# Kernel tuning notes

Hardware: AMD Instinct MI355X
Metric: run time of the kernel (lower is better)

Reference implementation:

```python
import jax, jax.numpy as jnp
import numpy as np

TOP_K = 2


def setup_inputs() -> dict:
    key = jax.random.key(0)
    ks = jax.random.split(key, 5)
    B, S, H, E, I = 2, 1024, 1024, 16, 1024
    scale = 1.0 / np.sqrt(H)
    return {
        "hidden_states": jax.random.normal(ks[0], (B, S, H), dtype=jnp.float32),
        "router_w": jax.random.normal(ks[1], (E, H), dtype=jnp.float32) * scale,   # nn.Linear(H,E).weight
        "gate_w": jax.random.normal(ks[2], (E, I, H), dtype=jnp.float32) * scale,  # per-expert Linear(H,I).weight
        "up_w": jax.random.normal(ks[3], (E, I, H), dtype=jnp.float32) * scale,
        "down_w": jax.random.normal(ks[4], (E, H, I), dtype=jnp.float32) * (1.0 / np.sqrt(I)),
    }


def reference(hidden_states, router_w, gate_w, up_w, down_w):
    orig_shape = hidden_states.shape
    x = hidden_states.reshape(-1, orig_shape[-1])  # [T, H]
    T = x.shape[0]
    E = router_w.shape[0]

    # Router: sigmoid -> top-k -> normalize
    logits = jnp.einsum("th,eh->te", x, router_w)           # [T, E]
    scores = jax.nn.sigmoid(logits)
    weights, indices = jax.lax.top_k(scores, TOP_K)         # [T, K]
    weights = weights / (weights.sum(axis=-1, keepdims=True) + 1e-20)

    # Dense per-token-per-expert combine weight (0 for unrouted pairs) ==
    # exact math of the torch gather/index_add loop.
    w_full = jnp.zeros((T, E), dtype=x.dtype).at[
        jnp.arange(T)[:, None], indices
    ].add(weights)                                          # [T, E]

    # Expert MLPs (SwiGLU) computed for all experts, zero-weighted combine.
    g = jax.nn.silu(jnp.einsum("th,eih->tei", x, gate_w))   # [T, E, I]
    u = jnp.einsum("th,eih->tei", x, up_w)                  # [T, E, I]
    out = jnp.einsum("te,tei,ehi->th", w_full, g * u, down_w)  # [T, H]
    return out.reshape(orig_shape)
```

## Files before the change

### kernel.cpp

```cpp
#include <hip/hip_runtime.h>
#include <stdint.h>

#define T_TOK 2048
#define H_DIM 1024
#define E_NUM 16
#define I_DIM 1024
#define TOTAL_ROWS (2 * T_TOK)
#define CPAD 16

typedef short bf16x8 __attribute__((ext_vector_type(8)));
typedef float f32x4 __attribute__((ext_vector_type(4)));

__device__ __forceinline__ void async_copy16(const void* g, void* l) {
  __builtin_amdgcn_global_load_lds(
      (const __attribute__((address_space(1))) void*)g,
      (__attribute__((address_space(3))) void*)l, 16, 0, 0);
}

__device__ __forceinline__ uint32_t f2bf(float f) {
  uint32_t u = __float_as_uint(f);
  return (u + 0x7FFFu + ((u >> 16) & 1u)) >> 16;
}
__device__ __forceinline__ uint32_t pk2bf(float lo, float hi) {
  return f2bf(lo) | (f2bf(hi) << 16);
}

__global__ __launch_bounds__(256) void router_kernel(
    const float* __restrict__ x, const float* __restrict__ rw,
    uint16_t* __restrict__ xbf, int* __restrict__ counts,
    int* __restrict__ tokens, float* __restrict__ wts) {
  const int t = blockIdx.x * 4 + (threadIdx.x >> 6);
  const int lane = threadIdx.x & 63;

  float4 xv[4];
  float acc[E_NUM];
#pragma unroll
  for (int e = 0; e < E_NUM; ++e) acc[e] = 0.f;

#pragma unroll
  for (int rep = 0; rep < 4; ++rep) {
    const int h0 = rep * 256 + lane * 4;
    xv[rep] = *(const float4*)(x + (size_t)t * H_DIM + h0);
    uint2 p;
    p.x = pk2bf(xv[rep].x, xv[rep].y);
    p.y = pk2bf(xv[rep].z, xv[rep].w);
    *(uint2*)(xbf + (size_t)t * H_DIM + h0) = p;
  }

#pragma unroll
  for (int e = 0; e < E_NUM; ++e) {
#pragma unroll
    for (int rep = 0; rep < 4; ++rep) {
      const float4 rv = *(const float4*)(rw + (size_t)e * H_DIM + rep * 256 + lane * 4);
      acc[e] += xv[rep].x * rv.x + xv[rep].y * rv.y + xv[rep].z * rv.z +
                xv[rep].w * rv.w;
    }
  }

#pragma unroll
  for (int e = 0; e < E_NUM; ++e) {
    float v = acc[e];
#pragma unroll
    for (int off = 32; off > 0; off >>= 1) v += __shfl_xor(v, off);
    acc[e] = v;
  }

  if (lane < 2) {
    float s[E_NUM];
#pragma unroll
    for (int e = 0; e < E_NUM; ++e) s[e] = 1.f / (1.f + expf(-acc[e]));
    int i1 = 0;
    float v1 = s[0];
#pragma unroll
    for (int e = 1; e < E_NUM; ++e)
      if (s[e] > v1) { v1 = s[e]; i1 = e; }
    int i2 = -1;
    float v2 = -1.f;
#pragma unroll
    for (int e = 0; e < E_NUM; ++e)
      if (e != i1 && s[e] > v2) { v2 = s[e]; i2 = e; }
    const float inv = 1.f / (v1 + v2 + 1e-20f);
    const int pe = (lane == 0) ? i1 : i2;
    const float pw = ((lane == 0) ? v1 : v2) * inv;
    const int slot = atomicAdd(&counts[pe * CPAD], 1);
    tokens[pe * T_TOK + slot] = t;
    wts[pe * T_TOK + slot] = pw;
  }
}

__global__ void offsets_kernel(const int* __restrict__ counts,
                               int* __restrict__ offsets) {
  if (threadIdx.x == 0) {
    int a = 0;
    for (int e = 0; e < E_NUM; ++e) {
      offsets[e] = a;
      a += counts[e * CPAD];
    }
    offsets[E_NUM] = a;
  }
}


__global__ __launch_bounds__(512, 4) void gemm1_kernel(
    const uint16_t* __restrict__ xbf, const float* __restrict__ gate,
    const float* __restrict__ up, const int* __restrict__ counts,
    const int* __restrict__ offsets, const int* __restrict__ tokens,
    const float* __restrict__ wts, uint16_t* __restrict__ hbuf) {
  const int e = blockIdx.z;
  const int count = counts[e * CPAD];
  const int m0 = blockIdx.y * 256;
  if (m0 >= count) return;
  const int n0 = blockIdx.x * 32;

  __shared__ __align__(16) uint16_t As[256 * 64];
  __shared__ __align__(16) uint16_t Bgs[32 * 64];
  __shared__ __align__(16) uint16_t Bus[32 * 64];
  __shared__ int tok_s[256];
  __shared__ float wt_s[256];

  const int tid = threadIdx.x;
  if (tid < 256) {
    const int slot = m0 + tid;
    int tk = 0;
    float w = 0.f;
    if (slot < count) {
      tk = tokens[e * T_TOK + slot];
      w = wts[e * T_TOK + slot];
    }
    tok_s[tid] = tk;
    wt_s[tid] = w;
  }
  __syncthreads();

  const uint16_t* a_g[4];
  uint16_t* a_l[4];
#pragma unroll
  for (int j = 0; j < 4; ++j) {
    const int c = j * 512 + tid;
    const int m = c >> 3;
    const int kq = (c & 7) ^ (m & 7);
    a_g[j] = xbf + (size_t)tok_s[m] * H_DIM + kq * 8;
    a_l[j] = As + c * 8;
  }
  const int bc = tid & 255;
  const int bm = bc >> 3;
  const int bkq = (bc & 7) ^ (bm & 7);
  const float* b_src =
      ((tid < 256) ? gate : up) + ((size_t)e * I_DIM + n0 + bm) * H_DIM + bkq * 8;
  uint16_t* b_dst = ((tid < 256) ? Bgs : Bus) + bc * 8;

  const int wave = tid >> 6, lane = tid & 63;
  const int wm = wave * 32;
  const int lc = lane & 15, lq = lane >> 4;
  const int l7 = lc & 7;

  f32x4 accg[2][2], accu[2][2];
  const f32x4 zero4 = {0.f, 0.f, 0.f, 0.f};
#pragma unroll
  for (int i = 0; i < 2; ++i)
#pragma unroll
    for (int j = 0; j < 2; ++j) {
      accg[i][j] = zero4;
      accu[i][j] = zero4;
    }

  int am[2], bn[2];
#pragma unroll
  for (int i = 0; i < 2; ++i) am[i] = (wm + i * 16 + lc) * 64;
#pragma unroll
  for (int i = 0; i < 2; ++i) bn[i] = (i * 16 + lc) * 64;

  float4 br0 = *(const float4*)b_src;
  float4 br1 = *(const float4*)(b_src + 4);

  for (int k0 = 0; k0 < H_DIM; k0 += 64) {
    __syncthreads();
#pragma unroll
    for (int j = 0; j < 4; ++j) async_copy16(a_g[j] + k0, a_l[j]);
    uint4 p;
    p.x = pk2bf(br0.x, br0.y);
    p.y = pk2bf(br0.z, br0.w);
    p.z = pk2bf(br1.x, br1.y);
    p.w = pk2bf(br1.z, br1.w);
    *(uint4*)b_dst = p;
    __syncthreads();
    if (k0 + 64 < H_DIM) {
      br0 = *(const float4*)(b_src + k0 + 64);
      br1 = *(const float4*)(b_src + k0 + 68);
    }

#pragma unroll
    for (int ks = 0; ks < 2; ++ks) {
      const int kswz = ((ks * 4 + lq) ^ l7) * 8;
      bf16x8 af[2], bg[2], bu[2];
#pragma unroll
      for (int i = 0; i < 2; ++i) af[i] = *(const bf16x8*)(As + am[i] + kswz);
#pragma unroll
      for (int i = 0; i < 2; ++i) {
        bg[i] = *(const bf16x8*)(Bgs + bn[i] + kswz);
        bu[i] = *(const bf16x8*)(Bus + bn[i] + kswz);
      }
#pragma unroll
      for (int im = 0; im < 2; ++im)
#pragma unroll
        for (int in = 0; in < 2; ++in) {
          accg[im][in] = __builtin_amdgcn_mfma_f32_16x16x32_bf16(
              af[im], bg[in], accg[im][in], 0, 0, 0);
          accu[im][in] = __builtin_amdgcn_mfma_f32_16x16x32_bf16(
              af[im], bu[in], accu[im][in], 0, 0, 0);
        }
    }
  }

  const int off_e = offsets[e];
#pragma unroll
  for (int im = 0; im < 2; ++im) {
#pragma unroll
    for (int r = 0; r < 4; ++r) {
      const int row = wm + im * 16 + lq * 4 + r;
      const int slot = m0 + row;
      if (slot < count) {
        const float w = wt_s[row];
        uint16_t* hrow = hbuf + (size_t)(off_e + slot) * I_DIM + n0;
#pragma unroll
        for (int in = 0; in < 2; ++in) {
          const float g = accg[im][in][r];
          const float u = accu[im][in][r];
          const float hv = g / (1.f + __expf(-g)) * u * w;
          hrow[in * 16 + lc] = (uint16_t)f2bf(hv);
        }
      }
    }
  }
}

__global__ __launch_bounds__(512, 4) void gemm2_kernel(
    const uint16_t* __restrict__ hbuf, const float* __restrict__ down,
    const int* __restrict__ counts, const int* __restrict__ offsets,
    const int* __restrict__ tokens, float* __restrict__ out) {
  const int e = blockIdx.z;
  const int count = counts[e * CPAD];
  const int m0 = blockIdx.y * 256;
  if (m0 >= count) return;
  const int n0 = blockIdx.x * 32;

  __shared__ __align__(16) uint16_t As[256 * 64];
  __shared__ __align__(16) uint16_t Bs[32 * 64];
  __shared__ int tok_s[256];

  const int tid = threadIdx.x;
  const int off_e = offsets[e];
  if (tid < 256) {
    const int slot = m0 + tid;
    tok_s[tid] = (slot < count) ? tokens[e * T_TOK + slot] : 0;
  }

  const uint16_t* a_g[4];
  uint16_t* a_l[4];
#pragma unroll
  for (int j = 0; j < 4; ++j) {
    const int c = j * 512 + tid;
    const int m = c >> 3;
    const int kq = (c & 7) ^ (m & 7);
    int r = off_e + m0 + m;
    if (r > TOTAL_ROWS - 1) r = TOTAL_ROWS - 1;
    a_g[j] = hbuf + (size_t)r * I_DIM + kq * 8;
    a_l[j] = As + c * 8;
  }
  const int bc = tid >> 1;
  const int half = tid & 1;
  const int bm = bc >> 3;
  const int bkq = (bc & 7) ^ (bm & 7);
  const float* d_g =
      down + ((size_t)e * H_DIM + n0 + bm) * I_DIM + bkq * 8 + half * 4;
  uint16_t* b_l = Bs + bc * 8 + half * 4;

  const int wave = tid >> 6, lane = tid & 63;
  const int wm = wave * 32;
  const int lc = lane & 15, lq = lane >> 4;
  const int l7 = lc & 7;

  f32x4 acc[2][2];
  const f32x4 zero4 = {0.f, 0.f, 0.f, 0.f};
#pragma unroll
  for (int i = 0; i < 2; ++i)
#pragma unroll
    for (int j = 0; j < 2; ++j) acc[i][j] = zero4;

  int am[2], bn[2];
#pragma unroll
  for (int i = 0; i < 2; ++i) am[i] = (wm + i * 16 + lc) * 64;
#pragma unroll
  for (int i = 0; i < 2; ++i) bn[i] = (i * 16 + lc) * 64;

  __syncthreads();

  float4 dr0 = *(const float4*)d_g;

  for (int k0 = 0; k0 < I_DIM; k0 += 64) {
    __syncthreads();
#pragma unroll
    for (int j = 0; j < 4; ++j) async_copy16(a_g[j] + k0, a_l[j]);
    uint2 p;
    p.x = pk2bf(dr0.x, dr0.y);
    p.y = pk2bf(dr0.z, dr0.w);
    *(uint2*)b_l = p;
    __syncthreads();
    if (k0 + 64 < I_DIM) {
      dr0 = *(const float4*)(d_g + k0 + 64);
    }

#pragma unroll
    for (int ks = 0; ks < 2; ++ks) {
      const int kswz = ((ks * 4 + lq) ^ l7) * 8;
      bf16x8 af[2], bf[2];
#pragma unroll
      for (int i = 0; i < 2; ++i) af[i] = *(const bf16x8*)(As + am[i] + kswz);
#pragma unroll
      for (int i = 0; i < 2; ++i) bf[i] = *(const bf16x8*)(Bs + bn[i] + kswz);
#pragma unroll
      for (int im = 0; im < 2; ++im)
#pragma unroll
        for (int in = 0; in < 2; ++in)
          acc[im][in] = __builtin_amdgcn_mfma_f32_16x16x32_bf16(
              af[im], bf[in], acc[im][in], 0, 0, 0);
    }
  }

#pragma unroll
  for (int im = 0; im < 2; ++im) {
#pragma unroll
    for (int r = 0; r < 4; ++r) {
      const int row = wm + im * 16 + lq * 4 + r;
      const int slot = m0 + row;
      if (slot < count) {
        float* orow = out + (size_t)tok_s[row] * H_DIM + n0;
#pragma unroll
        for (int in = 0; in < 2; ++in)
          atomicAdd(orow + in * 16 + lc, acc[im][in][r]);
      }
    }
  }
}

extern "C" void kernel_launch(void* const* d_in, const int* in_sizes, int n_in,
                              void* d_out, int out_size, void* d_ws,
                              size_t ws_size, hipStream_t stream) {
  const float* x = (const float*)d_in[0];
  const float* rw = (const float*)d_in[1];
  const float* gate = (const float*)d_in[2];
  const float* up = (const float*)d_in[3];
  const float* down = (const float*)d_in[4];
  float* out = (float*)d_out;

  uint8_t* ws = (uint8_t*)d_ws;
  int* counts = (int*)ws;
  int* offsets = (int*)(ws + 2048);
  int* tokens = (int*)(ws + 4096);
  float* wts = (float*)(ws + 4096 + 131072);
  uint16_t* xbf = (uint16_t*)(ws + 4096 + 262144);
  uint16_t* hbuf = (uint16_t*)(ws + 4096 + 262144 + 4194304);

  hipMemsetAsync(counts, 0, 2048, stream);
  hipMemsetAsync(out, 0, (size_t)out_size * sizeof(float), stream);

  router_kernel<<<512, 256, 0, stream>>>(x, rw, xbf, counts, tokens, wts);
  offsets_kernel<<<1, 64, 0, stream>>>(counts, offsets);
  gemm1_kernel<<<dim3(32, 8, 16), 512, 0, stream>>>(
      xbf, gate, up, counts, offsets, tokens, wts, hbuf);
  gemm2_kernel<<<dim3(32, 8, 16), 512, 0, stream>>>(hbuf, down, counts,
                                                    offsets, tokens, out);
}
```

Measured before the change: 287.0 us.

## Double-buffer LDS tiles and shrink GEMM blocks to 128 rows with 256 threads

Both expert GEMM kernels now keep two LDS buffers for the A and B tiles. The next k-slice's async copies and fp32 weight loads are issued before the MFMA loop on the current slice, which drops one barrier per iteration and overlaps loads with compute. Block size drops from 512 to 256 threads and the M tile from 256 to 128 rows, doubling the grid in y. Each thread now converts gate and up weights itself. The trade-off is that weight tiles are re-read by twice as many blocks, and LDS use per block changes.

```diff
diff --git a/kernel.cpp b/kernel.cpp
--- a/kernel.cpp
+++ b/kernel.cpp
@@ -101,25 +101,25 @@
 }
 
 
-__global__ __launch_bounds__(512, 4) void gemm1_kernel(
+__global__ __launch_bounds__(256, 3) void gemm1_kernel(
     const uint16_t* __restrict__ xbf, const float* __restrict__ gate,
     const float* __restrict__ up, const int* __restrict__ counts,
     const int* __restrict__ offsets, const int* __restrict__ tokens,
     const float* __restrict__ wts, uint16_t* __restrict__ hbuf) {
   const int e = blockIdx.z;
   const int count = counts[e * CPAD];
-  const int m0 = blockIdx.y * 256;
+  const int m0 = blockIdx.y * 128;
   if (m0 >= count) return;
   const int n0 = blockIdx.x * 32;
 
-  __shared__ __align__(16) uint16_t As[256 * 64];
-  __shared__ __align__(16) uint16_t Bgs[32 * 64];
-  __shared__ __align__(16) uint16_t Bus[32 * 64];
-  __shared__ int tok_s[256];
-  __shared__ float wt_s[256];
+  __shared__ __align__(16) uint16_t As[2][128 * 64];
+  __shared__ __align__(16) uint16_t Bgs[2][32 * 64];
+  __shared__ __align__(16) uint16_t Bus[2][32 * 64];
+  __shared__ int tok_s[128];
+  __shared__ float wt_s[128];
 
   const int tid = threadIdx.x;
-  if (tid < 256) {
+  if (tid < 128) {
     const int slot = m0 + tid;
     int tk = 0;
     float w = 0.f;
@@ -133,21 +133,20 @@
   __syncthreads();
 
   const uint16_t* a_g[4];
-  uint16_t* a_l[4];
+  int a_c[4];
 #pragma unroll
   for (int j = 0; j < 4; ++j) {
-    const int c = j * 512 + tid;
+    const int c = j * 256 + tid;
     const int m = c >> 3;
     const int kq = (c & 7) ^ (m & 7);
     a_g[j] = xbf + (size_t)tok_s[m] * H_DIM + kq * 8;
-    a_l[j] = As + c * 8;
-  }
-  const int bc = tid & 255;
-  const int bm = bc >> 3;
-  const int bkq = (bc & 7) ^ (bm & 7);
-  const float* b_src =
-      ((tid < 256) ? gate : up) + ((size_t)e * I_DIM + n0 + bm) * H_DIM + bkq * 8;
-  uint16_t* b_dst = ((tid < 256) ? Bgs : Bus) + bc * 8;
+    a_c[j] = c * 8;
+  }
+  const int bm = tid >> 3;
+  const int bkq = (tid & 7) ^ (bm & 7);
+  const float* g_g = gate + ((size_t)e * I_DIM + n0 + bm) * H_DIM + bkq * 8;
+  const float* u_g = up + ((size_t)e * I_DIM + n0 + bm) * H_DIM + bkq * 8;
+  const int b_c = tid * 8;
 
   const int wave = tid >> 6, lane = tid & 63;
   const int wm = wave * 32;
@@ -170,23 +169,39 @@
 #pragma unroll
   for (int i = 0; i < 2; ++i) bn[i] = (i * 16 + lc) * 64;
 
-  float4 br0 = *(const float4*)b_src;
-  float4 br1 = *(const float4*)(b_src + 4);
-
+#pragma unroll
+  for (int j = 0; j < 4; ++j) async_copy16(a_g[j], &As[0][a_c[j]]);
+  float4 g0 = *(const float4*)g_g;
+  float4 g1 = *(const float4*)(g_g + 4);
+  float4 u0 = *(const float4*)u_g;
+  float4 u1 = *(const float4*)(u_g + 4);
+  {
+    uint4 p;
+    p.x = pk2bf(g0.x, g0.y);
+    p.y = pk2bf(g0.z, g0.w);
+    p.z = pk2bf(g1.x, g1.y);
+    p.w = pk2bf(g1.z, g1.w);
+    *(uint4*)&Bgs[0][b_c] = p;
+    p.x = pk2bf(u0.x, u0.y);
+    p.y = pk2bf(u0.z, u0.w);
+    p.z = pk2bf(u1.x, u1.y);
+    p.w = pk2bf(u1.z, u1.w);
+    *(uint4*)&Bus[0][b_c] = p;
+  }
+  __syncthreads();
+
+  int cur = 0;
   for (int k0 = 0; k0 < H_DIM; k0 += 64) {
-    __syncthreads();
-#pragma unroll
-    for (int j = 0; j < 4; ++j) async_copy16(a_g[j] + k0, a_l[j]);
-    uint4 p;
-    p.x = pk2bf(br0.x, br0.y);
-    p.y = pk2bf(br0.z, br0.w);
-    p.z = pk2bf(br1.x, br1.y);
-    p.w = pk2bf(br1.z, br1.w);
-    *(uint4*)b_dst = p;
-    __syncthreads();
-    if (k0 + 64 < H_DIM) {
-      br0 = *(const float4*)(b_src + k0 + 64);
-      br1 = *(const float4*)(b_src + k0 + 68);
+    const int nxt = k0 + 64;
+    const bool more = (nxt < H_DIM);
+    if (more) {
+#pragma unroll
+      for (int j = 0; j < 4; ++j)
+        async_copy16(a_g[j] + nxt, &As[cur ^ 1][a_c[j]]);
+      g0 = *(const float4*)(g_g + nxt);
+      g1 = *(const float4*)(g_g + nxt + 4);
+      u0 = *(const float4*)(u_g + nxt);
+      u1 = *(const float4*)(u_g + nxt + 4);
     }
 
 #pragma unroll
@@ -194,11 +209,12 @@
       const int kswz = ((ks * 4 + lq) ^ l7) * 8;
       bf16x8 af[2], bg[2], bu[2];
 #pragma unroll
-      for (int i = 0; i < 2; ++i) af[i] = *(const bf16x8*)(As + am[i] + kswz);
+      for (int i = 0; i < 2; ++i)
+        af[i] = *(const bf16x8*)&As[cur][am[i] + kswz];
 #pragma unroll
       for (int i = 0; i < 2; ++i) {
-        bg[i] = *(const bf16x8*)(Bgs + bn[i] + kswz);
-        bu[i] = *(const bf16x8*)(Bus + bn[i] + kswz);
+        bg[i] = *(const bf16x8*)&Bgs[cur][bn[i] + kswz];
+        bu[i] = *(const bf16x8*)&Bus[cur][bn[i] + kswz];
       }
 #pragma unroll
       for (int im = 0; im < 2; ++im)
@@ -209,6 +225,22 @@
           accu[im][in] = __builtin_amdgcn_mfma_f32_16x16x32_bf16(
               af[im], bu[in], accu[im][in], 0, 0, 0);
         }
+    }
+
+    if (more) {
+      uint4 p;
+      p.x = pk2bf(g0.x, g0.y);
+      p.y = pk2bf(g0.z, g0.w);
+      p.z = pk2bf(g1.x, g1.y);
+      p.w = pk2bf(g1.z, g1.w);
+      *(uint4*)&Bgs[cur ^ 1][b_c] = p;
+      p.x = pk2bf(u0.x, u0.y);
+      p.y = pk2bf(u0.z, u0.w);
+      p.z = pk2bf(u1.x, u1.y);
+      p.w = pk2bf(u1.z, u1.w);
+      *(uint4*)&Bus[cur ^ 1][b_c] = p;
+      __syncthreads();
+      cur ^= 1;
     }
   }
 
@@ -234,46 +266,43 @@
   }
 }
 
-__global__ __launch_bounds__(512, 4) void gemm2_kernel(
+__global__ __launch_bounds__(256, 3) void gemm2_kernel(
     const uint16_t* __restrict__ hbuf, const float* __restrict__ down,
     const int* __restrict__ counts, const int* __restrict__ offsets,
     const int* __restrict__ tokens, float* __restrict__ out) {
   const int e = blockIdx.z;
   const int count = counts[e * CPAD];
-  const int m0 = blockIdx.y * 256;
+  const int m0 = blockIdx.y * 128;
   if (m0 >= count) return;
   const int n0 = blockIdx.x * 32;
 
-  __shared__ __align__(16) uint16_t As[256 * 64];
-  __shared__ __align__(16) uint16_t Bs[32 * 64];
-  __shared__ int tok_s[256];
+  __shared__ __align__(16) uint16_t As[2][128 * 64];
+  __shared__ __align__(16) uint16_t Bs[2][32 * 64];
+  __shared__ int tok_s[128];
 
   const int tid = threadIdx.x;
   const int off_e = offsets[e];
-  if (tid < 256) {
+  if (tid < 128) {
     const int slot = m0 + tid;
     tok_s[tid] = (slot < count) ? tokens[e * T_TOK + slot] : 0;
   }
 
   const uint16_t* a_g[4];
-  uint16_t* a_l[4];
+  int a_c[4];
 #pragma unroll
   for (int j = 0; j < 4; ++j) {
-    const int c = j * 512 + tid;
+    const int c = j * 256 + tid;
     const int m = c >> 3;
     const int kq = (c & 7) ^ (m & 7);
     int r = off_e + m0 + m;
     if (r > TOTAL_ROWS - 1) r = TOTAL_ROWS - 1;
     a_g[j] = hbuf + (size_t)r * I_DIM + kq * 8;
-    a_l[j] = As + c * 8;
-  }
-  const int bc = tid >> 1;
-  const int half = tid & 1;
-  const int bm = bc >> 3;
-  const int bkq = (bc & 7) ^ (bm & 7);
-  const float* d_g =
-      down + ((size_t)e * H_DIM + n0 + bm) * I_DIM + bkq * 8 + half * 4;
-  uint16_t* b_l = Bs + bc * 8 + half * 4;
+    a_c[j] = c * 8;
+  }
+  const int bm = tid >> 3;
+  const int bkq = (tid & 7) ^ (bm & 7);
+  const float* d_g = down + ((size_t)e * H_DIM + n0 + bm) * I_DIM + bkq * 8;
+  const int b_c = tid * 8;
 
   const int wave = tid >> 6, lane = tid & 63;
   const int wm = wave * 32;
@@ -293,21 +322,30 @@
 #pragma unroll
   for (int i = 0; i < 2; ++i) bn[i] = (i * 16 + lc) * 64;
 
+#pragma unroll
+  for (int j = 0; j < 4; ++j) async_copy16(a_g[j], &As[0][a_c[j]]);
+  float4 d0 = *(const float4*)d_g;
+  float4 d1 = *(const float4*)(d_g + 4);
+  {
+    uint4 p;
+    p.x = pk2bf(d0.x, d0.y);
+    p.y = pk2bf(d0.z, d0.w);
+    p.z = pk2bf(d1.x, d1.y);
+    p.w = pk2bf(d1.z, d1.w);
+    *(uint4*)&Bs[0][b_c] = p;
+  }
   __syncthreads();
 
-  float4 dr0 = *(const float4*)d_g;
-
+  int cur = 0;
   for (int k0 = 0; k0 < I_DIM; k0 += 64) {
-    __syncthreads();
-#pragma unroll
-    for (int j = 0; j < 4; ++j) async_copy16(a_g[j] + k0, a_l[j]);
-    uint2 p;
-    p.x = pk2bf(dr0.x, dr0.y);
-    p.y = pk2bf(dr0.z, dr0.w);
-    *(uint2*)b_l = p;
-    __syncthreads();
-    if (k0 + 64 < I_DIM) {
-      dr0 = *(const float4*)(d_g + k0 + 64);
+    const int nxt = k0 + 64;
+    const bool more = (nxt < I_DIM);
+    if (more) {
+#pragma unroll
+      for (int j = 0; j < 4; ++j)
+        async_copy16(a_g[j] + nxt, &As[cur ^ 1][a_c[j]]);
+      d0 = *(const float4*)(d_g + nxt);
+      d1 = *(const float4*)(d_g + nxt + 4);
     }
 
 #pragma unroll
@@ -315,15 +353,28 @@
       const int kswz = ((ks * 4 + lq) ^ l7) * 8;
       bf16x8 af[2], bf[2];
 #pragma unroll
-      for (int i = 0; i < 2; ++i) af[i] = *(const bf16x8*)(As + am[i] + kswz);
-#pragma unroll
-      for (int i = 0; i < 2; ++i) bf[i] = *(const bf16x8*)(Bs + bn[i] + kswz);
+      for (int i = 0; i < 2; ++i)
+        af[i] = *(const bf16x8*)&As[cur][am[i] + kswz];
+#pragma unroll
+      for (int i = 0; i < 2; ++i)
+        bf[i] = *(const bf16x8*)&Bs[cur][bn[i] + kswz];
 #pragma unroll
       for (int im = 0; im < 2; ++im)
 #pragma unroll
         for (int in = 0; in < 2; ++in)
           acc[im][in] = __builtin_amdgcn_mfma_f32_16x16x32_bf16(
               af[im], bf[in], acc[im][in], 0, 0, 0);
+    }
+
+    if (more) {
+      uint4 p;
+      p.x = pk2bf(d0.x, d0.y);
+      p.y = pk2bf(d0.z, d0.w);
+      p.z = pk2bf(d1.x, d1.y);
+      p.w = pk2bf(d1.z, d1.w);
+      *(uint4*)&Bs[cur ^ 1][b_c] = p;
+      __syncthreads();
+      cur ^= 1;
     }
   }
 
@@ -366,8 +417,8 @@
 
   router_kernel<<<512, 256, 0, stream>>>(x, rw, xbf, counts, tokens, wts);
   offsets_kernel<<<1, 64, 0, stream>>>(counts, offsets);
-  gemm1_kernel<<<dim3(32, 8, 16), 512, 0, stream>>>(
+  gemm1_kernel<<<dim3(32, 16, 16), 256, 0, stream>>>(
       xbf, gate, up, counts, offsets, tokens, wts, hbuf);
-  gemm2_kernel<<<dim3(32, 8, 16), 512, 0, stream>>>(hbuf, down, counts,
-                                                    offsets, tokens, out);
-}
+  gemm2_kernel<<<dim3(32, 16, 16), 256, 0, stream>>>(hbuf, down, counts,
+                                                     offsets, tokens, out);
+}
```

New measurement: 299.5 us. +4.4%, slower.

## Double-buffer expert GEMMs with 128x64 tiles and replace output atomics with combine kernel

Applied to the files above, without the earlier changes.

Both expert GEMM kernels now use 256-thread blocks with 128x64 tiles, double-buffered LDS, and register prefetch of the fp32 weights two K-steps ahead. Explicit waitcnt and sched_barrier fencing overlaps global loads with MFMA work. The second GEMM now writes per-slot rows to a scratch buffer instead of doing atomicAdd into the output. A new combine kernel sums each token's two expert rows, which also removes the output memset. This trades extra scratch traffic and one more launch for no atomics and better latency hiding.

```diff
diff --git a/kernel.cpp b/kernel.cpp
--- a/kernel.cpp
+++ b/kernel.cpp
@@ -25,10 +25,20 @@
   return f2bf(lo) | (f2bf(hi) << 16);
 }
 
+#define WS_COUNTS 0
+#define WS_OFFSETS 2048
+#define WS_ROWS 4096
+#define WS_TOKENS 20480
+#define WS_WTS 151552
+#define WS_XBF 294912
+#define WS_HBUF (WS_XBF + 4194304)
+#define WS_OBUF (WS_HBUF + 8388608)
+
 __global__ __launch_bounds__(256) void router_kernel(
     const float* __restrict__ x, const float* __restrict__ rw,
     uint16_t* __restrict__ xbf, int* __restrict__ counts,
-    int* __restrict__ tokens, float* __restrict__ wts) {
+    int* __restrict__ tokens, float* __restrict__ wts,
+    int* __restrict__ rows) {
   const int t = blockIdx.x * 4 + (threadIdx.x >> 6);
   const int lane = threadIdx.x & 63;
 
@@ -51,7 +61,8 @@
   for (int e = 0; e < E_NUM; ++e) {
 #pragma unroll
     for (int rep = 0; rep < 4; ++rep) {
-      const float4 rv = *(const float4*)(rw + (size_t)e * H_DIM + rep * 256 + lane * 4);
+      const float4 rv =
+          *(const float4*)(rw + (size_t)e * H_DIM + rep * 256 + lane * 4);
       acc[e] += xv[rep].x * rv.x + xv[rep].y * rv.y + xv[rep].z * rv.z +
                 xv[rep].w * rv.w;
     }
@@ -85,6 +96,7 @@
     const int slot = atomicAdd(&counts[pe * CPAD], 1);
     tokens[pe * T_TOK + slot] = t;
     wts[pe * T_TOK + slot] = pw;
+    rows[t * 2 + lane] = pe * 4096 + slot;
   }
 }
 
@@ -100,26 +112,27 @@
   }
 }
 
-
-__global__ __launch_bounds__(512, 4) void gemm1_kernel(
+#define FENCE() __builtin_amdgcn_sched_barrier(0)
+
+__global__ __launch_bounds__(256, 2) void gemm1_kernel(
     const uint16_t* __restrict__ xbf, const float* __restrict__ gate,
     const float* __restrict__ up, const int* __restrict__ counts,
     const int* __restrict__ offsets, const int* __restrict__ tokens,
     const float* __restrict__ wts, uint16_t* __restrict__ hbuf) {
   const int e = blockIdx.z;
   const int count = counts[e * CPAD];
-  const int m0 = blockIdx.y * 256;
+  const int m0 = blockIdx.y * 128;
   if (m0 >= count) return;
-  const int n0 = blockIdx.x * 32;
-
-  __shared__ __align__(16) uint16_t As[256 * 64];
-  __shared__ __align__(16) uint16_t Bgs[32 * 64];
-  __shared__ __align__(16) uint16_t Bus[32 * 64];
-  __shared__ int tok_s[256];
-  __shared__ float wt_s[256];
+  const int n0 = blockIdx.x * 64;
+
+  __shared__ __align__(16) uint16_t As[2][128 * 64];
+  __shared__ __align__(16) uint16_t Bgs[2][64 * 64];
+  __shared__ __align__(16) uint16_t Bus[2][64 * 64];
+  __shared__ int tok_s[128];
+  __shared__ float wt_s[128];
 
   const int tid = threadIdx.x;
-  if (tid < 256) {
+  if (tid < 128) {
     const int slot = m0 + tid;
     int tk = 0;
     float w = 0.f;
@@ -133,84 +146,149 @@
   __syncthreads();
 
   const uint16_t* a_g[4];
-  uint16_t* a_l[4];
+  int a_c[4];
 #pragma unroll
   for (int j = 0; j < 4; ++j) {
-    const int c = j * 512 + tid;
+    const int c = j * 256 + tid;
     const int m = c >> 3;
     const int kq = (c & 7) ^ (m & 7);
     a_g[j] = xbf + (size_t)tok_s[m] * H_DIM + kq * 8;
-    a_l[j] = As + c * 8;
-  }
-  const int bc = tid & 255;
-  const int bm = bc >> 3;
-  const int bkq = (bc & 7) ^ (bm & 7);
-  const float* b_src =
-      ((tid < 256) ? gate : up) + ((size_t)e * I_DIM + n0 + bm) * H_DIM + bkq * 8;
-  uint16_t* b_dst = ((tid < 256) ? Bgs : Bus) + bc * 8;
+    a_c[j] = c * 8;
+  }
+  const int bm = tid >> 3;
+  const int bkq = (tid & 7) ^ (bm & 7);
+  const float* gp0 = gate + ((size_t)e * I_DIM + n0 + bm) * H_DIM + bkq * 8;
+  const float* gp1 = gp0 + 32 * H_DIM;
+  const float* uq0 = up + ((size_t)e * I_DIM + n0 + bm) * H_DIM + bkq * 8;
+  const float* uq1 = uq0 + 32 * H_DIM;
+  const int bc0 = tid * 8, bc1 = (tid + 256) * 8;
 
   const int wave = tid >> 6, lane = tid & 63;
   const int wm = wave * 32;
   const int lc = lane & 15, lq = lane >> 4;
   const int l7 = lc & 7;
 
-  f32x4 accg[2][2], accu[2][2];
+  f32x4 accg[2][4], accu[2][4];
   const f32x4 zero4 = {0.f, 0.f, 0.f, 0.f};
 #pragma unroll
   for (int i = 0; i < 2; ++i)
 #pragma unroll
-    for (int j = 0; j < 2; ++j) {
+    for (int j = 0; j < 4; ++j) {
       accg[i][j] = zero4;
       accu[i][j] = zero4;
     }
 
-  int am[2], bn[2];
+  int am[2], bn[4];
 #pragma unroll
   for (int i = 0; i < 2; ++i) am[i] = (wm + i * 16 + lc) * 64;
 #pragma unroll
-  for (int i = 0; i < 2; ++i) bn[i] = (i * 16 + lc) * 64;
-
-  float4 br0 = *(const float4*)b_src;
-  float4 br1 = *(const float4*)(b_src + 4);
-
-  for (int k0 = 0; k0 < H_DIM; k0 += 64) {
-    __syncthreads();
-#pragma unroll
-    for (int j = 0; j < 4; ++j) async_copy16(a_g[j] + k0, a_l[j]);
-    uint4 p;
-    p.x = pk2bf(br0.x, br0.y);
-    p.y = pk2bf(br0.z, br0.w);
-    p.z = pk2bf(br1.x, br1.y);
-    p.w = pk2bf(br1.z, br1.w);
-    *(uint4*)b_dst = p;
-    __syncthreads();
-    if (k0 + 64 < H_DIM) {
-      br0 = *(const float4*)(b_src + k0 + 64);
-      br1 = *(const float4*)(b_src + k0 + 68);
-    }
-
-#pragma unroll
-    for (int ks = 0; ks < 2; ++ks) {
-      const int kswz = ((ks * 4 + lq) ^ l7) * 8;
-      bf16x8 af[2], bg[2], bu[2];
-#pragma unroll
-      for (int i = 0; i < 2; ++i) af[i] = *(const bf16x8*)(As + am[i] + kswz);
-#pragma unroll
-      for (int i = 0; i < 2; ++i) {
-        bg[i] = *(const bf16x8*)(Bgs + bn[i] + kswz);
-        bu[i] = *(const bf16x8*)(Bus + bn[i] + kswz);
-      }
-#pragma unroll
-      for (int im = 0; im < 2; ++im)
-#pragma unroll
-        for (int in = 0; in < 2; ++in) {
-          accg[im][in] = __builtin_amdgcn_mfma_f32_16x16x32_bf16(
-              af[im], bg[in], accg[im][in], 0, 0, 0);
-          accu[im][in] = __builtin_amdgcn_mfma_f32_16x16x32_bf16(
-              af[im], bu[in], accu[im][in], 0, 0, 0);
-        }
-    }
-  }
+  for (int i = 0; i < 4; ++i) bn[i] = (i * 16 + lc) * 64;
+
+  float4 bA[8];
+  float4 bB[8];
+
+#define G1_STAGE(BUF, KT)                                                 \
+  {                                                                       \
+    const int ko_ = (KT)*64;                                              \
+    _Pragma("unroll") for (int j = 0; j < 4; ++j)                         \
+        async_copy16(a_g[j] + ko_, &As[BUF][a_c[j]]);                     \
+  }
+
+#define G1_LOADB(KT, v)                                                   \
+  v[0] = *(const float4*)(gp0 + (KT)*64);                                 \
+  v[1] = *(const float4*)(gp0 + (KT)*64 + 4);                             \
+  v[2] = *(const float4*)(gp1 + (KT)*64);                                 \
+  v[3] = *(const float4*)(gp1 + (KT)*64 + 4);                             \
+  v[4] = *(const float4*)(uq0 + (KT)*64);                                 \
+  v[5] = *(const float4*)(uq0 + (KT)*64 + 4);                             \
+  v[6] = *(const float4*)(uq1 + (KT)*64);                                 \
+  v[7] = *(const float4*)(uq1 + (KT)*64 + 4);
+
+#define G1_WRITEB(BUF, v)                                                 \
+  {                                                                       \
+    uint4 p;                                                              \
+    p.x = pk2bf(v[0].x, v[0].y); p.y = pk2bf(v[0].z, v[0].w);             \
+    p.z = pk2bf(v[1].x, v[1].y); p.w = pk2bf(v[1].z, v[1].w);             \
+    *(uint4*)&Bgs[BUF][bc0] = p;                                          \
+    p.x = pk2bf(v[2].x, v[2].y); p.y = pk2bf(v[2].z, v[2].w);             \
+    p.z = pk2bf(v[3].x, v[3].y); p.w = pk2bf(v[3].z, v[3].w);             \
+    *(uint4*)&Bgs[BUF][bc1] = p;                                          \
+    p.x = pk2bf(v[4].x, v[4].y); p.y = pk2bf(v[4].z, v[4].w);             \
+    p.z = pk2bf(v[5].x, v[5].y); p.w = pk2bf(v[5].z, v[5].w);             \
+    *(uint4*)&Bus[BUF][bc0] = p;                                          \
+    p.x = pk2bf(v[6].x, v[6].y); p.y = pk2bf(v[6].z, v[6].w);             \
+    p.z = pk2bf(v[7].x, v[7].y); p.w = pk2bf(v[7].z, v[7].w);             \
+    *(uint4*)&Bus[BUF][bc1] = p;                                          \
+  }
+
+#define G1_COMPUTE(CB)                                                    \
+  _Pragma("unroll") for (int ks = 0; ks < 2; ++ks) {                      \
+    const int kswz = ((ks * 4 + lq) ^ l7) * 8;                            \
+    bf16x8 af[2], bg[4], bu[4];                                           \
+    _Pragma("unroll") for (int i = 0; i < 2; ++i) af[i] =                 \
+        *(const bf16x8*)&As[CB][am[i] + kswz];                            \
+    _Pragma("unroll") for (int i = 0; i < 4; ++i) {                       \
+      bg[i] = *(const bf16x8*)&Bgs[CB][bn[i] + kswz];                     \
+      bu[i] = *(const bf16x8*)&Bus[CB][bn[i] + kswz];                     \
+    }                                                                     \
+    _Pragma("unroll") for (int im = 0; im < 2; ++im)                      \
+        _Pragma("unroll") for (int in = 0; in < 4; ++in) {                \
+      accg[im][in] = __builtin_amdgcn_mfma_f32_16x16x32_bf16(             \
+          af[im], bg[in], accg[im][in], 0, 0, 0);                         \
+      accu[im][in] = __builtin_amdgcn_mfma_f32_16x16x32_bf16(             \
+          af[im], bu[in], accu[im][in], 0, 0, 0);                         \
+    }                                                                     \
+  }
+
+  G1_STAGE(0, 0)
+  G1_LOADB(0, bA)
+  G1_LOADB(1, bB)
+  asm volatile("s_waitcnt vmcnt(8)" ::: "memory");
+  FENCE();
+  G1_WRITEB(0, bA)
+  asm volatile("s_waitcnt lgkmcnt(0)" ::: "memory");
+  FENCE();
+  __builtin_amdgcn_s_barrier();
+  FENCE();
+
+  int cur = 0;
+#pragma unroll 1
+  for (int t2 = 0; t2 < 7; ++t2) {
+    const int t = t2 * 2;
+    G1_STAGE(cur ^ 1, t + 1)
+    G1_LOADB(t + 2, bA)
+    G1_COMPUTE(cur)
+    asm volatile("s_waitcnt vmcnt(12)" ::: "memory");
+    FENCE();
+    G1_WRITEB(cur ^ 1, bB)
+    asm volatile("s_waitcnt vmcnt(8) lgkmcnt(0)" ::: "memory");
+    FENCE();
+    __builtin_amdgcn_s_barrier();
+    FENCE();
+    cur ^= 1;
+    G1_STAGE(cur ^ 1, t + 2)
+    G1_LOADB(t + 3, bB)
+    G1_COMPUTE(cur)
+    asm volatile("s_waitcnt vmcnt(12)" ::: "memory");
+    FENCE();
+    G1_WRITEB(cur ^ 1, bA)
+    asm volatile("s_waitcnt vmcnt(8) lgkmcnt(0)" ::: "memory");
+    FENCE();
+    __builtin_amdgcn_s_barrier();
+    FENCE();
+    cur ^= 1;
+  }
+  G1_STAGE(cur ^ 1, 15)
+  G1_COMPUTE(cur)
+  asm volatile("s_waitcnt vmcnt(4)" ::: "memory");
+  FENCE();
+  G1_WRITEB(cur ^ 1, bB)
+  asm volatile("s_waitcnt vmcnt(0) lgkmcnt(0)" ::: "memory");
+  FENCE();
+  __builtin_amdgcn_s_barrier();
+  FENCE();
+  cur ^= 1;
+  G1_COMPUTE(cur)
 
   const int off_e = offsets[e];
 #pragma unroll
@@ -223,7 +301,7 @@
         const float w = wt_s[row];
         uint16_t* hrow = hbuf + (size_t)(off_e + slot) * I_DIM + n0;
 #pragma unroll
-        for (int in = 0; in < 2; ++in) {
+        for (int in = 0; in < 4; ++in) {
           const float g = accg[im][in][r];
           const float u = accu[im][in][r];
           const float hv = g / (1.f + __expf(-g)) * u * w;
@@ -234,98 +312,148 @@
   }
 }
 
-__global__ __launch_bounds__(512, 4) void gemm2_kernel(
+__global__ __launch_bounds__(256, 3) void gemm2_kernel(
     const uint16_t* __restrict__ hbuf, const float* __restrict__ down,
     const int* __restrict__ counts, const int* __restrict__ offsets,
-    const int* __restrict__ tokens, float* __restrict__ out) {
+    float* __restrict__ obuf) {
   const int e = blockIdx.z;
   const int count = counts[e * CPAD];
-  const int m0 = blockIdx.y * 256;
+  const int m0 = blockIdx.y * 128;
   if (m0 >= count) return;
-  const int n0 = blockIdx.x * 32;
-
-  __shared__ __align__(16) uint16_t As[256 * 64];
-  __shared__ __align__(16) uint16_t Bs[32 * 64];
-  __shared__ int tok_s[256];
+  const int n0 = blockIdx.x * 64;
+
+  __shared__ __align__(16) uint16_t As[2][128 * 64];
+  __shared__ __align__(16) uint16_t Bs[2][64 * 64];
 
   const int tid = threadIdx.x;
   const int off_e = offsets[e];
-  if (tid < 256) {
-    const int slot = m0 + tid;
-    tok_s[tid] = (slot < count) ? tokens[e * T_TOK + slot] : 0;
-  }
 
   const uint16_t* a_g[4];
-  uint16_t* a_l[4];
+  int a_c[4];
 #pragma unroll
   for (int j = 0; j < 4; ++j) {
-    const int c = j * 512 + tid;
+    const int c = j * 256 + tid;
     const int m = c >> 3;
     const int kq = (c & 7) ^ (m & 7);
     int r = off_e + m0 + m;
     if (r > TOTAL_ROWS - 1) r = TOTAL_ROWS - 1;
     a_g[j] = hbuf + (size_t)r * I_DIM + kq * 8;
-    a_l[j] = As + c * 8;
-  }
-  const int bc = tid >> 1;
-  const int half = tid & 1;
-  const int bm = bc >> 3;
-  const int bkq = (bc & 7) ^ (bm & 7);
-  const float* d_g =
-      down + ((size_t)e * H_DIM + n0 + bm) * I_DIM + bkq * 8 + half * 4;
-  uint16_t* b_l = Bs + bc * 8 + half * 4;
+    a_c[j] = c * 8;
+  }
+  const int bm = tid >> 3;
+  const int bkq = (tid & 7) ^ (bm & 7);
+  const float* dp0 = down + ((size_t)e * H_DIM + n0 + bm) * I_DIM + bkq * 8;
+  const float* dp1 = dp0 + 32 * I_DIM;
+  const int bc0 = tid * 8, bc1 = (tid + 256) * 8;
 
   const int wave = tid >> 6, lane = tid & 63;
   const int wm = wave * 32;
   const int lc = lane & 15, lq = lane >> 4;
   const int l7 = lc & 7;
 
-  f32x4 acc[2][2];
+  f32x4 acc[2][4];
   const f32x4 zero4 = {0.f, 0.f, 0.f, 0.f};
 #pragma unroll
   for (int i = 0; i < 2; ++i)
 #pragma unroll
-    for (int j = 0; j < 2; ++j) acc[i][j] = zero4;
-
-  int am[2], bn[2];
+    for (int j = 0; j < 4; ++j) acc[i][j] = zero4;
+
+  int am[2], bn[4];
 #pragma unroll
   for (int i = 0; i < 2; ++i) am[i] = (wm + i * 16 + lc) * 64;
 #pragma unroll
-  for (int i = 0; i < 2; ++i) bn[i] = (i * 16 + lc) * 64;
-
-  __syncthreads();
-
-  float4 dr0 = *(const float4*)d_g;
-
-  for (int k0 = 0; k0 < I_DIM; k0 += 64) {
-    __syncthreads();
-#pragma unroll
-    for (int j = 0; j < 4; ++j) async_copy16(a_g[j] + k0, a_l[j]);
-    uint2 p;
-    p.x = pk2bf(dr0.x, dr0.y);
-    p.y = pk2bf(dr0.z, dr0.w);
-    *(uint2*)b_l = p;
-    __syncthreads();
-    if (k0 + 64 < I_DIM) {
-      dr0 = *(const float4*)(d_g + k0 + 64);
-    }
-
-#pragma unroll
-    for (int ks = 0; ks < 2; ++ks) {
-      const int kswz = ((ks * 4 + lq) ^ l7) * 8;
-      bf16x8 af[2], bf[2];
-#pragma unroll
-      for (int i = 0; i < 2; ++i) af[i] = *(const bf16x8*)(As + am[i] + kswz);
-#pragma unroll
-      for (int i = 0; i < 2; ++i) bf[i] = *(const bf16x8*)(Bs + bn[i] + kswz);
-#pragma unroll
-      for (int im = 0; im < 2; ++im)
-#pragma unroll
-        for (int in = 0; in < 2; ++in)
-          acc[im][in] = __builtin_amdgcn_mfma_f32_16x16x32_bf16(
-              af[im], bf[in], acc[im][in], 0, 0, 0);
-    }
-  }
+  for (int i = 0; i < 4; ++i) bn[i] = (i * 16 + lc) * 64;
+
+  float4 dA[4];
+  float4 dB[4];
+
+#define G2_STAGE(BUF, KT)                                                 \
+  {                                                                       \
+    const int ko_ = (KT)*64;                                              \
+    _Pragma("unroll") for (int j = 0; j < 4; ++j)                         \
+        async_copy16(a_g[j] + ko_, &As[BUF][a_c[j]]);                     \
+  }
+
+#define G2_LOADB(KT, v)                                                   \
+  v[0] = *(const float4*)(dp0 + (KT)*64);                                 \
+  v[1] = *(const float4*)(dp0 + (KT)*64 + 4);                             \
+  v[2] = *(const float4*)(dp1 + (KT)*64);                                 \
+  v[3] = *(const float4*)(dp1 + (KT)*64 + 4);
+
+#define G2_WRITEB(BUF, v)                                                 \
+  {                                                                       \
+    uint4 p;                                                              \
+    p.x = pk2bf(v[0].x, v[0].y); p.y = pk2bf(v[0].z, v[0].w);             \
+    p.z = pk2bf(v[1].x, v[1].y); p.w = pk2bf(v[1].z, v[1].w);             \
+    *(uint4*)&Bs[BUF][bc0] = p;                                           \
+    p.x = pk2bf(v[2].x, v[2].y); p.y = pk2bf(v[2].z, v[2].w);             \
+    p.z = pk2bf(v[3].x, v[3].y); p.w = pk2bf(v[3].z, v[3].w);             \
+    *(uint4*)&Bs[BUF][bc1] = p;                                           \
+  }
+
+#define G2_COMPUTE(CB)                                                    \
+  _Pragma("unroll") for (int ks = 0; ks < 2; ++ks) {                      \
+    const int kswz = ((ks * 4 + lq) ^ l7) * 8;                            \
+    bf16x8 af[2], bf[4];                                                  \
+    _Pragma("unroll") for (int i = 0; i < 2; ++i) af[i] =                 \
+        *(const bf16x8*)&As[CB][am[i] + kswz];                            \
+    _Pragma("unroll") for (int i = 0; i < 4; ++i) bf[i] =                 \
+        *(const bf16x8*)&Bs[CB][bn[i] + kswz];                            \
+    _Pragma("unroll") for (int im = 0; im < 2; ++im)                      \
+        _Pragma("unroll") for (int in = 0; in < 4; ++in) acc[im][in] =    \
+            __builtin_amdgcn_mfma_f32_16x16x32_bf16(af[im], bf[in],       \
+                                                    acc[im][in], 0, 0, 0);\
+  }
+
+  G2_STAGE(0, 0)
+  G2_LOADB(0, dA)
+  G2_LOADB(1, dB)
+  asm volatile("s_waitcnt vmcnt(4)" ::: "memory");
+  FENCE();
+  G2_WRITEB(0, dA)
+  asm volatile("s_waitcnt lgkmcnt(0)" ::: "memory");
+  FENCE();
+  __builtin_amdgcn_s_barrier();
+  FENCE();
+
+  int cur = 0;
+#pragma unroll 1
+  for (int t2 = 0; t2 < 7; ++t2) {
+    const int t = t2 * 2;
+    G2_STAGE(cur ^ 1, t + 1)
+    G2_LOADB(t + 2, dA)
+    G2_COMPUTE(cur)
+    asm volatile("s_waitcnt vmcnt(8)" ::: "memory");
+    FENCE();
+    G2_WRITEB(cur ^ 1, dB)
+    asm volatile("s_waitcnt vmcnt(4) lgkmcnt(0)" ::: "memory");
+    FENCE();
+    __builtin_amdgcn_s_barrier();
+    FENCE();
+    cur ^= 1;
+    G2_STAGE(cur ^ 1, t + 2)
+    G2_LOADB(t + 3, dB)
+    G2_COMPUTE(cur)
+    asm volatile("s_waitcnt vmcnt(8)" ::: "memory");
+    FENCE();
+    G2_WRITEB(cur ^ 1, dA)
+    asm volatile("s_waitcnt vmcnt(4) lgkmcnt(0)" ::: "memory");
+    FENCE();
+    __builtin_amdgcn_s_barrier();
+    FENCE();
+    cur ^= 1;
+  }
+  G2_STAGE(cur ^ 1, 15)
+  G2_COMPUTE(cur)
+  asm volatile("s_waitcnt vmcnt(4)" ::: "memory");
+  FENCE();
+  G2_WRITEB(cur ^ 1, dB)
+  asm volatile("s_waitcnt vmcnt(0) lgkmcnt(0)" ::: "memory");
+  FENCE();
+  __builtin_amdgcn_s_barrier();
+  FENCE();
+  cur ^= 1;
+  G2_COMPUTE(cur)
 
 #pragma unroll
   for (int im = 0; im < 2; ++im) {
@@ -334,13 +462,32 @@
       const int row = wm + im * 16 + lq * 4 + r;
       const int slot = m0 + row;
       if (slot < count) {
-        float* orow = out + (size_t)tok_s[row] * H_DIM + n0;
-#pragma unroll
-        for (int in = 0; in < 2; ++in)
-          atomicAdd(orow + in * 16 + lc, acc[im][in][r]);
+        float* orow = obuf + (size_t)(off_e + slot) * H_DIM + n0;
+#pragma unroll
+        for (int in = 0; in < 4; ++in)
+          orow[in * 16 + lc] = acc[im][in][r];
       }
     }
   }
+}
+
+__global__ __launch_bounds__(256) void combine_kernel(
+    const float* __restrict__ obuf, const int* __restrict__ rows,
+    const int* __restrict__ offsets, float* __restrict__ out) {
+  const int t = blockIdx.x;
+  const int c = threadIdx.x * 4;
+  const int e0 = rows[t * 2 + 0];
+  const int e1 = rows[t * 2 + 1];
+  const size_t r0 = offsets[e0 >> 12] + (e0 & 4095);
+  const size_t r1 = offsets[e1 >> 12] + (e1 & 4095);
+  const float4 a = *(const float4*)(obuf + r0 * H_DIM + c);
+  const float4 b = *(const float4*)(obuf + r1 * H_DIM + c);
+  float4 o;
+  o.x = a.x + b.x;
+  o.y = a.y + b.y;
+  o.z = a.z + b.z;
+  o.w = a.w + b.w;
+  *(float4*)(out + (size_t)t * H_DIM + c) = o;
 }
 
 extern "C" void kernel_launch(void* const* d_in, const int* in_sizes, int n_in,
@@ -354,20 +501,23 @@
   float* out = (float*)d_out;
 
   uint8_t* ws = (uint8_t*)d_ws;
-  int* counts = (int*)ws;
-  int* offsets = (int*)(ws + 2048);
-  int* tokens = (int*)(ws + 4096);
-  float* wts = (float*)(ws + 4096 + 131072);
-  uint16_t* xbf = (uint16_t*)(ws + 4096 + 262144);
-  uint16_t* hbuf = (uint16_t*)(ws + 4096 + 262144 + 4194304);
+  int* counts = (int*)(ws + WS_COUNTS);
+  int* offsets = (int*)(ws + WS_OFFSETS);
+  int* rows = (int*)(ws + WS_ROWS);
+  int* tokens = (int*)(ws + WS_TOKENS);
+  float* wts = (float*)(ws + WS_WTS);
+  uint16_t* xbf = (uint16_t*)(ws + WS_XBF);
+  uint16_t* hbuf = (uint16_t*)(ws + WS_HBUF);
+  float* obuf = (float*)(ws + WS_OBUF);
 
   hipMemsetAsync(counts, 0, 2048, stream);
-  hipMemsetAsync(out, 0, (size_t)out_size * sizeof(float), stream);
-
-  router_kernel<<<512, 256, 0, stream>>>(x, rw, xbf, counts, tokens, wts);
+
+  router_kernel<<<512, 256, 0, stream>>>(x, rw, xbf, counts, tokens, wts,
+                                         rows);
   offsets_kernel<<<1, 64, 0, stream>>>(counts, offsets);
-  gemm1_kernel<<<dim3(32, 8, 16), 512, 0, stream>>>(
+  gemm1_kernel<<<dim3(16, 16, 16), 256, 0, stream>>>(
       xbf, gate, up, counts, offsets, tokens, wts, hbuf);
-  gemm2_kernel<<<dim3(32, 8, 16), 512, 0, stream>>>(hbuf, down, counts,
-                                                    offsets, tokens, out);
-}
+  gemm2_kernel<<<dim3(16, 16, 16), 256, 0, stream>>>(hbuf, down, counts,
+                                                     offsets, obuf);
+  combine_kernel<<<T_TOK, 256, 0, stream>>>(obuf, rows, offsets, out);
+}
```

Measured after the change: 280.0 us. 1.02x faster.
